# Performance work log

Hardware: AMD Instinct MI355X
Metric: run time of the kernel (lower is better)

Reference implementation:

```python
import jax, jax.numpy as jnp
import numpy as np

T = 4096          # total packed tokens (4 docs x 1024)
NUM_DOCS = 4
H = 16            # n_heads
D = 64            # head_dim == v_head_dim
TOPK = 64         # per-token top-k KV selection (<= min doc len)


def setup_inputs() -> dict:
    key = jax.random.key(0)
    kq, kk, kv, ki, ks = jax.random.split(key, 5)
    q = jax.random.normal(kq, (T, H, D), dtype=jnp.float32)
    k = jax.random.normal(kk, (T, H, D), dtype=jnp.float32)
    v = jax.random.normal(kv, (T, H, D), dtype=jnp.float32)
    # 4 equal-length documents of 1024 tokens
    cu_seqlens = (jnp.arange(NUM_DOCS + 1, dtype=jnp.int32) * (T // NUM_DOCS))
    # global top-k indices; reference clamps them into the owning document
    topk_indices = jax.random.randint(ki, (T, TOPK), 0, T, dtype=jnp.int32)
    # selector scores in (0,1), like indexer softmax outputs
    topk_scores = jax.random.uniform(ks, (T, TOPK), dtype=jnp.float32)
    return {
        "q_packed": q,
        "k_packed": k,
        "v_packed": v,
        "cu_seqlens": cu_seqlens,
        "topk_indices": topk_indices,
        "topk_scores": topk_scores,
    }


def reference(q_packed, k_packed, v_packed, cu_seqlens, topk_indices, topk_scores):
    total_tokens, n_heads, head_dim = q_packed.shape
    scale = head_dim ** -0.5

    # Per-token document assignment (vectorized replacement for the doc loop).
    tok = jnp.arange(total_tokens, dtype=cu_seqlens.dtype)
    seg = jnp.searchsorted(cu_seqlens[1:], tok, side="right")  # (T,) doc id
    start = cu_seqlens[seg]                                    # (T,)
    seq_len = cu_seqlens[seg + 1] - start                      # (T,)

    # Localize and clamp top-k indices into the owning document, then
    # convert back to global packed indices for gathering.
    local = jnp.clip(topk_indices - start[:, None], 0, (seq_len - 1)[:, None])
    gidx = start[:, None] + local                              # (T, K)

    k_gathered = k_packed[gidx]   # (T, K, H, D)
    v_gathered = v_packed[gidx]   # (T, K, H, D)

    # q . k_sel, softmax over the k selected keys
    scores = jnp.einsum("thd,tkhd->thk", q_packed, k_gathered) * scale
    w = jax.nn.softmax(scores, axis=-1)                        # (T, H, K)

    # Modulate by selector scores (head-shared) and renormalize.
    w = w * topk_scores[:, None, :]
    w = w / (jnp.sum(w, axis=-1, keepdims=True) + 1e-12)

    out = jnp.einsum("thk,tkhd->thd", w, v_gathered)           # (T, H, D)
    return out
```

## Files before the change

kernel.cpp:

```cpp
#include <hip/hip_runtime.h>


#define T_TOK 4096
#define NH    16
#define HD    64
#define KSEL  64

__global__ __launch_bounds__(256, 4) void dsa_sparse_attn(
    const float* __restrict__ qM,
    const float* __restrict__ kM,
    const float* __restrict__ vM,
    const int*   __restrict__ cu,
    const int*   __restrict__ tidx,
    const float* __restrict__ tsc,
    float*       __restrict__ out,
    int num_docs)
{
    const int wave = threadIdx.x >> 6;
    const int lane = threadIdx.x & 63;
    const int gid  = (blockIdx.x << 2) + wave;
    const int t    = gid >> 4;
    const int h    = gid & (NH - 1);

    __shared__ __align__(8) float2 s_wg[4][KSEL];

    int seg = 0;
    for (int i = 1; i < num_docs; ++i)
        if (t >= cu[i]) seg = i;
    const int start = cu[seg];
    const int len   = cu[seg + 1] - start;

    int idx = tidx[t * KSEL + lane];
    int loc = idx - start;
    loc = loc < 0 ? 0 : loc;
    loc = loc > len - 1 ? len - 1 : loc;
    const int g = start + loc;

    const int laneCol = lane & 3;
    const int laneRow = lane >> 2;

    const float4* qv = (const float4*)(qM + gid * HD);
    float4 q4[4];
    #pragma unroll
    for (int j = 0; j < 4; ++j)
        q4[j] = qv[j * 4 + laneCol];

    const float4* kf4 = (const float4*)kM;
    float score = 0.f;

    #pragma unroll
    for (int rg = 0; rg < 4; ++rg) {
        const int row  = rg * 16 + laneRow;
        const int grow = __shfl(g, row, 64);
        const int base = (grow * NH + h) * (HD / 4) + laneCol;
        float p = 0.f;
        #pragma unroll
        for (int j = 0; j < 4; ++j) {
            const float4 k4 = kf4[base + j * 4];
            p = fmaf(q4[j].x, k4.x, p);
            p = fmaf(q4[j].y, k4.y, p);
            p = fmaf(q4[j].z, k4.z, p);
            p = fmaf(q4[j].w, k4.w, p);
        }
        p += __shfl_xor(p, 1, 64);
        p += __shfl_xor(p, 2, 64);
        const float got = __shfl(p, (lane & 15) << 2, 64);
        if (rg == (lane >> 4)) score = got;
    }
    score *= 0.125f;

    float m = score;
    #pragma unroll
    for (int off = 32; off; off >>= 1)
        m = fmaxf(m, __shfl_xor(m, off, 64));
    const float e = __expf(score - m);
    const float p = e * tsc[t * KSEL + lane];
    float S1 = e, S2 = p;
    #pragma unroll
    for (int off = 32; off; off >>= 1) {
        S1 += __shfl_xor(S1, off, 64);
        S2 += __shfl_xor(S2, off, 64);
    }
    const float w = p / (S2 + 1e-12f * S1);

    s_wg[wave][lane] = make_float2(w, __int_as_float(g));
    __syncthreads();

    const int laneQ = lane >> 4;
    const int laneC = lane & 15;
    const float4* vf4 = (const float4*)vM;

    float4 acc = make_float4(0.f, 0.f, 0.f, 0.f);
    #pragma unroll 4
    for (int i = 0; i < 16; ++i) {
        const float2 wg = s_wg[wave][i * 4 + laneQ];
        const int   gg = __float_as_int(wg.y);
        const float wk = wg.x;
        const float4 v4 = vf4[(gg * NH + h) * (HD / 4) + laneC];
        acc.x = fmaf(wk, v4.x, acc.x);
        acc.y = fmaf(wk, v4.y, acc.y);
        acc.z = fmaf(wk, v4.z, acc.z);
        acc.w = fmaf(wk, v4.w, acc.w);
    }
    #pragma unroll
    for (int off = 16; off <= 32; off <<= 1) {
        acc.x += __shfl_xor(acc.x, off, 64);
        acc.y += __shfl_xor(acc.y, off, 64);
        acc.z += __shfl_xor(acc.z, off, 64);
        acc.w += __shfl_xor(acc.w, off, 64);
    }
    if (laneQ == 0)
        ((float4*)(out + gid * HD))[laneC] = acc;
}

extern "C" void kernel_launch(void* const* d_in, const int* in_sizes, int n_in,
                              void* d_out, int out_size, void* d_ws, size_t ws_size,
                              hipStream_t stream) {
    const float* q   = (const float*)d_in[0];
    const float* k   = (const float*)d_in[1];
    const float* v   = (const float*)d_in[2];
    const int*   cu  = (const int*)d_in[3];
    const int*   ti  = (const int*)d_in[4];
    const float* ts  = (const float*)d_in[5];
    float*       out = (float*)d_out;

    const int num_docs = in_sizes[3] - 1;
    const int total_waves = T_TOK * NH;
    dim3 grid(total_waves / 4), block(256);
    hipLaunchKernelGGL(dsa_sparse_attn, grid, block, 0, stream,
                       q, k, v, cu, ti, ts, out, num_docs);
}
```

Baseline: 158.1 us.

## Prefetch all K and V gathers into registers up front and drop LDS weight exchange

Each wave now issues all of its K and V row gathers (32 float4 per lane) at the start, before the QK dot products, so V loads overlap the score and softmax computation instead of being serialized after it. The weights are broadcast with wave shuffles rather than through shared memory, which removes the LDS buffer and the block-wide __syncthreads. Holding 32 float4 in registers raises VGPR pressure considerably, and the minimum-occupancy hint in launch_bounds is dropped, so fewer waves may be resident per SIMD.

```diff
diff --git a/kernel.cpp b/kernel.cpp
--- a/kernel.cpp
+++ b/kernel.cpp
@@ -6,7 +6,7 @@
 #define HD    64
 #define KSEL  64
 
-__global__ __launch_bounds__(256, 4) void dsa_sparse_attn(
+__global__ __launch_bounds__(256) void dsa_sparse_attn(
     const float* __restrict__ qM,
     const float* __restrict__ kM,
     const float* __restrict__ vM,
@@ -22,8 +22,6 @@
     const int t    = gid >> 4;
     const int h    = gid & (NH - 1);
 
-    __shared__ __align__(8) float2 s_wg[4][KSEL];
-
     int seg = 0;
     for (int i = 1; i < num_docs; ++i)
         if (t >= cu[i]) seg = i;
@@ -35,9 +33,37 @@
     loc = loc < 0 ? 0 : loc;
     loc = loc > len - 1 ? len - 1 : loc;
     const int g = start + loc;
+    const float sc = tsc[t * KSEL + lane];
 
     const int laneCol = lane & 3;
     const int laneRow = lane >> 2;
+    const int laneQ   = lane >> 4;
+    const int laneC   = lane & 15;
+
+    const float4* kf4 = (const float4*)kM;
+    const float4* vf4 = (const float4*)vM;
+
+    int gk[4];
+    #pragma unroll
+    for (int rg = 0; rg < 4; ++rg)
+        gk[rg] = __shfl(g, rg * 16 + laneRow, 64);
+    int gv[16];
+    #pragma unroll
+    for (int i = 0; i < 16; ++i)
+        gv[i] = __shfl(g, i * 4 + laneQ, 64);
+
+    float4 kreg[16];
+    #pragma unroll
+    for (int rg = 0; rg < 4; ++rg) {
+        const int base = (gk[rg] * NH + h) * (HD / 4) + laneCol;
+        #pragma unroll
+        for (int j = 0; j < 4; ++j)
+            kreg[rg * 4 + j] = kf4[base + j * 4];
+    }
+    float4 vreg[16];
+    #pragma unroll
+    for (int i = 0; i < 16; ++i)
+        vreg[i] = vf4[(gv[i] * NH + h) * (HD / 4) + laneC];
 
     const float4* qv = (const float4*)(qM + gid * HD);
     float4 q4[4];
@@ -45,18 +71,13 @@
     for (int j = 0; j < 4; ++j)
         q4[j] = qv[j * 4 + laneCol];
 
-    const float4* kf4 = (const float4*)kM;
     float score = 0.f;
-
     #pragma unroll
     for (int rg = 0; rg < 4; ++rg) {
-        const int row  = rg * 16 + laneRow;
-        const int grow = __shfl(g, row, 64);
-        const int base = (grow * NH + h) * (HD / 4) + laneCol;
         float p = 0.f;
         #pragma unroll
         for (int j = 0; j < 4; ++j) {
-            const float4 k4 = kf4[base + j * 4];
+            const float4 k4 = kreg[rg * 4 + j];
             p = fmaf(q4[j].x, k4.x, p);
             p = fmaf(q4[j].y, k4.y, p);
             p = fmaf(q4[j].z, k4.z, p);
@@ -74,7 +95,7 @@
     for (int off = 32; off; off >>= 1)
         m = fmaxf(m, __shfl_xor(m, off, 64));
     const float e = __expf(score - m);
-    const float p = e * tsc[t * KSEL + lane];
+    const float p = e * sc;
     float S1 = e, S2 = p;
     #pragma unroll
     for (int off = 32; off; off >>= 1) {
@@ -83,24 +104,14 @@
     }
     const float w = p / (S2 + 1e-12f * S1);
 
-    s_wg[wave][lane] = make_float2(w, __int_as_float(g));
-    __syncthreads();
-
-    const int laneQ = lane >> 4;
-    const int laneC = lane & 15;
-    const float4* vf4 = (const float4*)vM;
-
     float4 acc = make_float4(0.f, 0.f, 0.f, 0.f);
-    #pragma unroll 4
+    #pragma unroll
     for (int i = 0; i < 16; ++i) {
-        const float2 wg = s_wg[wave][i * 4 + laneQ];
-        const int   gg = __float_as_int(wg.y);
-        const float wk = wg.x;
-        const float4 v4 = vf4[(gg * NH + h) * (HD / 4) + laneC];
-        acc.x = fmaf(wk, v4.x, acc.x);
-        acc.y = fmaf(wk, v4.y, acc.y);
-        acc.z = fmaf(wk, v4.z, acc.z);
-        acc.w = fmaf(wk, v4.w, acc.w);
+        const float wk = __shfl(w, i * 4 + laneQ, 64);
+        acc.x = fmaf(wk, vreg[i].x, acc.x);
+        acc.y = fmaf(wk, vreg[i].y, acc.y);
+        acc.z = fmaf(wk, vreg[i].z, acc.z);
+        acc.w = fmaf(wk, vreg[i].w, acc.w);
     }
     #pragma unroll
     for (int off = 16; off <= 32; off <<= 1) {
```

After: 157.8 us. About the same (-0.2%).

## Convert K/V to fp16 in a pre-pass and remap blocks for XCD locality

Applied to the files above, without the earlier changes.

Adds a conversion kernel that writes K and V as fp16 into workspace, so the attention kernel's random gathers fetch half the bytes. The block index is remapped so each XCD works on a fixed set of head slices and a quarter of the tokens, which should improve L2 reuse of the gathered rows. The weight/index broadcast moves from LDS plus a __syncthreads to shuffles, and the V accumulation is restructured so each lane holds eight fp16 values. The conversion pass reads all of K and V every call, and fp16 K/V lowers precision.

```diff
diff --git a/kernel.cpp b/kernel.cpp
--- a/kernel.cpp
+++ b/kernel.cpp
@@ -1,28 +1,67 @@
 #include <hip/hip_runtime.h>
+#include <hip/hip_fp16.h>
 
 
 #define T_TOK 4096
 #define NH    16
 #define HD    64
 #define KSEL  64
+#define KV_ELEMS (T_TOK * NH * HD)
 
-__global__ __launch_bounds__(256, 4) void dsa_sparse_attn(
-    const float* __restrict__ qM,
-    const float* __restrict__ kM,
-    const float* __restrict__ vM,
-    const int*   __restrict__ cu,
-    const int*   __restrict__ tidx,
-    const float* __restrict__ tsc,
-    float*       __restrict__ out,
+__global__ __launch_bounds__(256) void cvt_fp16(
+    const float4* __restrict__ kM, const float4* __restrict__ vM,
+    uint2* __restrict__ kH, uint2* __restrict__ vH)
+{
+    const int n4 = KV_ELEMS / 4;
+    const int i  = blockIdx.x * blockDim.x + threadIdx.x;
+    const bool isK = i < n4;
+    const float4 f = isK ? kM[i] : vM[i - n4];
+    __half2 lo = __floats2half2_rn(f.x, f.y);
+    __half2 hi = __floats2half2_rn(f.z, f.w);
+    uint2 u;
+    u.x = *(const unsigned int*)&lo;
+    u.y = *(const unsigned int*)&hi;
+    if (isK) kH[i] = u; else vH[i - n4] = u;
+}
+
+__device__ __forceinline__ float dot8(const float4 kc,
+                                      const float4 q0, const float4 q1)
+{
+    const __half2* h2 = (const __half2*)&kc;
+    const float2 a = __half22float2(h2[0]);
+    const float2 b = __half22float2(h2[1]);
+    const float2 c = __half22float2(h2[2]);
+    const float2 d = __half22float2(h2[3]);
+    float p = 0.f;
+    p = fmaf(a.x, q0.x, p); p = fmaf(a.y, q0.y, p);
+    p = fmaf(b.x, q0.z, p); p = fmaf(b.y, q0.w, p);
+    p = fmaf(c.x, q1.x, p); p = fmaf(c.y, q1.y, p);
+    p = fmaf(d.x, q1.z, p); p = fmaf(d.y, q1.w, p);
+    return p;
+}
+
+__global__ __launch_bounds__(256) void dsa_sparse_attn(
+    const float*  __restrict__ qM,
+    const __half* __restrict__ kH,
+    const __half* __restrict__ vH,
+    const int*    __restrict__ cu,
+    const int*    __restrict__ tidx,
+    const float*  __restrict__ tsc,
+    float*        __restrict__ out,
     int num_docs)
 {
     const int wave = threadIdx.x >> 6;
     const int lane = threadIdx.x & 63;
-    const int gid  = (blockIdx.x << 2) + wave;
-    const int t    = gid >> 4;
-    const int h    = gid & (NH - 1);
 
-    __shared__ __align__(8) float2 s_wg[4][KSEL];
+    const int b            = blockIdx.x;
+    const int xcd          = b & 7;
+    const int j            = b >> 3;
+    const int token_block  = j & 255;
+    const int slice_within = j >> 8;
+    const int s            = xcd + (slice_within << 3);
+    const int h            = s & (NH - 1);
+    const int t            = (s >> 4) * (T_TOK / 4) + token_block * 4 + wave;
+    const int gid          = t * NH + h;
 
     int seg = 0;
     for (int i = 1; i < num_docs; ++i)
@@ -35,33 +74,27 @@
     loc = loc < 0 ? 0 : loc;
     loc = loc > len - 1 ? len - 1 : loc;
     const int g = start + loc;
+    const float sc = tsc[t * KSEL + lane];
 
     const int laneCol = lane & 3;
     const int laneRow = lane >> 2;
 
     const float4* qv = (const float4*)(qM + gid * HD);
-    float4 q4[4];
-    #pragma unroll
-    for (int j = 0; j < 4; ++j)
-        q4[j] = qv[j * 4 + laneCol];
+    const float4 qA0 = qv[laneCol * 2];
+    const float4 qA1 = qv[laneCol * 2 + 1];
+    const float4 qB0 = qv[8 + laneCol * 2];
+    const float4 qB1 = qv[8 + laneCol * 2 + 1];
 
-    const float4* kf4 = (const float4*)kM;
+    const float4* kf = (const float4*)kH;
     float score = 0.f;
-
     #pragma unroll
     for (int rg = 0; rg < 4; ++rg) {
         const int row  = rg * 16 + laneRow;
         const int grow = __shfl(g, row, 64);
-        const int base = (grow * NH + h) * (HD / 4) + laneCol;
-        float p = 0.f;
-        #pragma unroll
-        for (int j = 0; j < 4; ++j) {
-            const float4 k4 = kf4[base + j * 4];
-            p = fmaf(q4[j].x, k4.x, p);
-            p = fmaf(q4[j].y, k4.y, p);
-            p = fmaf(q4[j].z, k4.z, p);
-            p = fmaf(q4[j].w, k4.w, p);
-        }
+        const int base = (grow * NH + h) * 8;
+        const float4 kA = kf[base + laneCol];
+        const float4 kB = kf[base + 4 + laneCol];
+        float p = dot8(kA, qA0, qA1) + dot8(kB, qB0, qB1);
         p += __shfl_xor(p, 1, 64);
         p += __shfl_xor(p, 2, 64);
         const float got = __shfl(p, (lane & 15) << 2, 64);
@@ -74,7 +107,7 @@
     for (int off = 32; off; off >>= 1)
         m = fmaxf(m, __shfl_xor(m, off, 64));
     const float e = __expf(score - m);
-    const float p = e * tsc[t * KSEL + lane];
+    const float p = e * sc;
     float S1 = e, S2 = p;
     #pragma unroll
     for (int off = 32; off; off >>= 1) {
@@ -83,34 +116,42 @@
     }
     const float w = p / (S2 + 1e-12f * S1);
 
-    s_wg[wave][lane] = make_float2(w, __int_as_float(g));
-    __syncthreads();
+    const int laneC8 = lane & 7;
+    const int laneQ8 = lane >> 3;
+    const float4* vf = (const float4*)vH;
 
-    const int laneQ = lane >> 4;
-    const int laneC = lane & 15;
-    const float4* vf4 = (const float4*)vM;
-
-    float4 acc = make_float4(0.f, 0.f, 0.f, 0.f);
-    #pragma unroll 4
-    for (int i = 0; i < 16; ++i) {
-        const float2 wg = s_wg[wave][i * 4 + laneQ];
-        const int   gg = __float_as_int(wg.y);
-        const float wk = wg.x;
-        const float4 v4 = vf4[(gg * NH + h) * (HD / 4) + laneC];
-        acc.x = fmaf(wk, v4.x, acc.x);
-        acc.y = fmaf(wk, v4.y, acc.y);
-        acc.z = fmaf(wk, v4.z, acc.z);
-        acc.w = fmaf(wk, v4.w, acc.w);
+    float acc[8] = {0.f, 0.f, 0.f, 0.f, 0.f, 0.f, 0.f, 0.f};
+    #pragma unroll
+    for (int i = 0; i < 8; ++i) {
+        const int row = i * 8 + laneQ8;
+        const float wk = __shfl(w, row, 64);
+        const int   gg = __shfl(g, row, 64);
+        const float4 vc = vf[(gg * NH + h) * 8 + laneC8];
+        const __half2* h2 = (const __half2*)&vc;
+        const float2 a = __half22float2(h2[0]);
+        const float2 bq = __half22float2(h2[1]);
+        const float2 c = __half22float2(h2[2]);
+        const float2 d = __half22float2(h2[3]);
+        acc[0] = fmaf(wk, a.x,  acc[0]);
+        acc[1] = fmaf(wk, a.y,  acc[1]);
+        acc[2] = fmaf(wk, bq.x, acc[2]);
+        acc[3] = fmaf(wk, bq.y, acc[3]);
+        acc[4] = fmaf(wk, c.x,  acc[4]);
+        acc[5] = fmaf(wk, c.y,  acc[5]);
+        acc[6] = fmaf(wk, d.x,  acc[6]);
+        acc[7] = fmaf(wk, d.y,  acc[7]);
     }
     #pragma unroll
-    for (int off = 16; off <= 32; off <<= 1) {
-        acc.x += __shfl_xor(acc.x, off, 64);
-        acc.y += __shfl_xor(acc.y, off, 64);
-        acc.z += __shfl_xor(acc.z, off, 64);
-        acc.w += __shfl_xor(acc.w, off, 64);
+    for (int off = 8; off <= 32; off <<= 1) {
+        #pragma unroll
+        for (int ee = 0; ee < 8; ++ee)
+            acc[ee] += __shfl_xor(acc[ee], off, 64);
     }
-    if (laneQ == 0)
-        ((float4*)(out + gid * HD))[laneC] = acc;
+    if (laneQ8 == 0) {
+        float4* op = (float4*)(out + gid * HD + laneC8 * 8);
+        op[0] = make_float4(acc[0], acc[1], acc[2], acc[3]);
+        op[1] = make_float4(acc[4], acc[5], acc[6], acc[7]);
+    }
 }
 
 extern "C" void kernel_launch(void* const* d_in, const int* in_sizes, int n_in,
@@ -123,10 +164,18 @@
     const int*   ti  = (const int*)d_in[4];
     const float* ts  = (const float*)d_in[5];
     float*       out = (float*)d_out;
+    const int num_docs = in_sizes[3] - 1;
 
-    const int num_docs = in_sizes[3] - 1;
+    __half* kH = (__half*)d_ws;
+    __half* vH = kH + KV_ELEMS;
+
+    const int n4 = KV_ELEMS / 4;
+    hipLaunchKernelGGL(cvt_fp16, dim3(2 * n4 / 256), dim3(256), 0, stream,
+                       (const float4*)k, (const float4*)v,
+                       (uint2*)kH, (uint2*)vH);
+
     const int total_waves = T_TOK * NH;
-    dim3 grid(total_waves / 4), block(256);
-    hipLaunchKernelGGL(dsa_sparse_attn, grid, block, 0, stream,
-                       q, k, v, cu, ti, ts, out, num_docs);
+    hipLaunchKernelGGL(dsa_sparse_attn, dim3(total_waves / 4), dim3(256), 0,
+                       stream, q, (const __half*)kH, (const __half*)vH,
+                       cu, ti, ts, out, num_docs);
 }
```

After: 152.6 us. 3.5% less time.
